# Kernel optimization log

Hardware: AMD Instinct MI355X
Metric: run time of the kernel (lower is better)

## Reference

```python
import jax, jax.numpy as jnp
import numpy as np
import math

N = 100000          # nodes
E = 3200000         # edges
F_IN = 500          # num_features
HID = 64            # hidden
C = 64              # num_classes
K = 5               # trig frequencies
OMEGA = 1.0
D = 10              # Taylor order / diffusion hops


def _taylor_coeffs():
    # cos/sin Taylor coefficient tables, [K, D+1] (static, fp64 then cast)
    x = (np.arange(1, K + 1) * OMEGA * np.pi)[:, None].astype(np.float64)
    cosc = np.zeros((K, D + 1), np.float64)
    sinc = np.zeros((K, D + 1), np.float64)
    even = np.arange(0, D + 1, 2)
    cosc[:, ::2] = ((-1.0) ** (even // 2)) * x ** even / np.array([math.factorial(int(o)) for o in even], np.float64)
    odd = np.arange(1, D + 1, 2)
    sinc[:, 1::2] = ((-1.0) ** ((odd - 1) // 2)) * x ** odd / np.array([math.factorial(int(o)) for o in odd], np.float64)
    return jnp.asarray(sinc, jnp.float32), jnp.asarray(cosc, jnp.float32)

SINC, COSC = _taylor_coeffs()


def setup_inputs() -> dict:
    key = jax.random.key(0)
    ks = jax.random.split(key, 8)
    feature = jax.random.normal(ks[0], (N, F_IN), dtype=jnp.float32)
    edges = jax.random.randint(ks[1], (2, E), 0, N, dtype=jnp.int64)
    W1 = jax.random.normal(ks[2], (F_IN, HID), dtype=jnp.float32) * (1.0 / np.sqrt(F_IN))
    b1 = jnp.zeros((HID,), jnp.float32)
    W2 = jax.random.normal(ks[3], (HID, C), dtype=jnp.float32) * (1.0 / np.sqrt(HID))
    b2 = jnp.zeros((C,), jnp.float32)
    xav = np.sqrt(2.0 / (1 + K))  # xavier_normal for (1, K)
    alpha = jax.random.normal(ks[4], (1, K), dtype=jnp.float32) * xav
    beta = jax.random.normal(ks[5], (1, K), dtype=jnp.float32) * xav
    return {"feature": feature, "edges": edges, "W1": W1, "b1": b1,
            "W2": W2, "b2": b2, "alpha": alpha, "beta": beta}


def reference(feature, edges, W1, b1, W2, b2, alpha, beta):
    # dropout is identity in eval mode
    x = jnp.maximum(feature @ W1 + b1, 0.0)   # lin1 + relu
    x = x @ W2 + b2                           # lin2 -> [N, C]

    # ---- Trigo_prop.__norm__: sym-normalized Laplacian, rescale, self-loops -1 ----
    src, dst = edges[0], edges[1]
    not_loop = src != dst                     # remove_self_loops
    deg = jax.ops.segment_sum(jnp.where(not_loop, 1.0, 0.0).astype(x.dtype), src, num_segments=N)
    dinv = jnp.where(deg > 0, jax.lax.rsqrt(deg), 0.0)
    w_off = jnp.where(not_loop, -(dinv[src] * dinv[dst]), 0.0)   # off-diag of L_sym
    # Laplacian diagonal entries are all 1 -> lambda_max = 2*max(all weights)
    lam = 2.0 * jnp.maximum(jnp.max(w_off), 1.0)
    s = 2.0 / lam
    w_off = w_off * s
    diag = s * 1.0 - 1.0                      # scaled diag(1) plus appended -1 self-loop

    # ---- D-hop Taylor-weighted diffusion ----
    coeff = (alpha @ SINC + beta @ COSC)[0]   # [D+1]
    Tx = x
    hidden = coeff[0] * Tx
    for d in range(1, D + 1):                 # fixed small D, unrolled
        Tx = jax.ops.segment_sum(w_off[:, None] * Tx[src], dst, num_segments=N) + diag * Tx
        hidden = hidden + coeff[d] * Tx
    out = hidden + x
    return jax.nn.log_softmax(out, axis=1)
```

## Files before the change

### kernel.cpp

```cpp
#include <hip/hip_runtime.h>
#include <math.h>

#define NN 100000
#define FIN 500
#define HIDN 64
#define KF 5
#define DORD 10

typedef unsigned short ushort_t;

struct Tables { float sinc[KF][DORD+1]; float cosc[KF][DORD+1]; };

__device__ inline float bl(unsigned u) { return __uint_as_float(u << 16); }
__device__ inline float bh(unsigned u) { return __uint_as_float(u & 0xffff0000u); }
__device__ inline unsigned short bf16_rne(float x) {
    unsigned u = __float_as_uint(x);
    return (unsigned short)((u + 0x7fffu + ((u >> 16) & 1u)) >> 16);
}
__device__ inline unsigned pack_bf16x2(float a, float b) {
    return (unsigned)bf16_rne(a) | ((unsigned)bf16_rne(b) << 16);
}

__global__ void coeff_kernel(const float* __restrict__ alpha, const float* __restrict__ beta,
                             Tables tb, float* __restrict__ coeff) {
    int d = threadIdx.x;
    if (d <= DORD) {
        float c = 0.f;
        #pragma unroll
        for (int k = 0; k < KF; ++k)
            c += alpha[k] * tb.sinc[k][d] + beta[k] * tb.cosc[k][d];
        coeff[d] = c;
    }
}

#define CHUNK 4096

__global__ __launch_bounds__(256) void hist_kernel(
    const int* __restrict__ src, const int* __restrict__ dst,
    int* __restrict__ histD, int* __restrict__ histS, int E, int nb) {
    __shared__ int hD[512];
    __shared__ int hS[512];
    for (int i = threadIdx.x; i < 512; i += 256) { hD[i] = 0; hS[i] = 0; }
    __syncthreads();
    int base = blockIdx.x * CHUNK;
    int end = base + CHUNK; if (end > E) end = E;
    for (int e = base + threadIdx.x; e < end; e += 256) {
        int s = src[e], d = dst[e];
        if (s != d) {
            atomicAdd(&hD[d >> 8], 1);
            atomicAdd(&hS[s >> 8], 1);
        }
    }
    __syncthreads();
    size_t ro = (size_t)blockIdx.x * 512;
    for (int i = threadIdx.x; i < nb; i += 256) {
        histD[ro + i] = hD[i];
        histS[ro + i] = hS[i];
    }
}

__global__ __launch_bounds__(512) void scanA_kernel(
    int* __restrict__ histD, int* __restrict__ histS,
    int* __restrict__ totD, int* __restrict__ totS, int nchunk, int nb) {
    __shared__ int tmp[512];
    int x = blockIdx.x;
    int* hist; int* tot; int b;
    if (x < nb) { hist = histD; tot = totD; b = x; }
    else        { hist = histS; tot = totS; b = x - nb; }
    int t = threadIdx.x;
    int carry = 0;
    for (int c0 = 0; c0 < nchunk; c0 += 512) {
        int c = c0 + t;
        tmp[t] = (c < nchunk) ? hist[(size_t)c * 512 + b] : 0;
        __syncthreads();
        for (int off = 1; off < 512; off <<= 1) {
            int add = (t >= off) ? tmp[t - off] : 0;
            __syncthreads();
            tmp[t] += add;
            __syncthreads();
        }
        if (c < nchunk) hist[(size_t)c * 512 + b] = carry + ((t > 0) ? tmp[t - 1] : 0);
        carry += tmp[511];
        __syncthreads();
    }
    if (t == 0) tot[b] = carry;
}

__global__ __launch_bounds__(512) void scanB_kernel(
    const int* __restrict__ totD, const int* __restrict__ totS,
    int* __restrict__ offD, int* __restrict__ offS, int nb) {
    __shared__ int tmp[512];
    int t = threadIdx.x;
    tmp[t] = (t < nb) ? totD[t] : 0;
    __syncthreads();
    for (int off = 1; off < 512; off <<= 1) {
        int add = (t >= off) ? tmp[t - off] : 0;
        __syncthreads();
        tmp[t] += add;
        __syncthreads();
    }
    if (t < nb) offD[t] = (t > 0) ? tmp[t - 1] : 0;
    if (t == nb - 1) offD[nb] = tmp[t];
    __syncthreads();
    tmp[t] = (t < nb) ? totS[t] : 0;
    __syncthreads();
    for (int off = 1; off < 512; off <<= 1) {
        int add = (t >= off) ? tmp[t - off] : 0;
        __syncthreads();
        tmp[t] += add;
        __syncthreads();
    }
    if (t < nb) offS[t] = (t > 0) ? tmp[t - 1] : 0;
    if (t == nb - 1) offS[nb] = tmp[t];
}

__global__ __launch_bounds__(256) void scatter_kernel(
    const int* __restrict__ src, const int* __restrict__ dst,
    const int* __restrict__ histD, const int* __restrict__ histS,
    const int* __restrict__ offD, const int* __restrict__ offS,
    unsigned* __restrict__ binned, unsigned char* __restrict__ srcbin, int E, int nb) {
    __shared__ int cD[512];
    __shared__ int cS[512];
    size_t ro = (size_t)blockIdx.x * 512;
    for (int i = threadIdx.x; i < nb; i += 256) {
        cD[i] = offD[i] + histD[ro + i];
        cS[i] = offS[i] + histS[ro + i];
    }
    __syncthreads();
    int base = blockIdx.x * CHUNK;
    int end = base + CHUNK; if (end > E) end = E;
    for (int e = base + threadIdx.x; e < end; e += 256) {
        int s = src[e], d = dst[e];
        if (s != d) {
            int pD = atomicAdd(&cD[d >> 8], 1);
            binned[pD] = (unsigned)s | ((unsigned)(d & 255) << 24);
            int pS = atomicAdd(&cS[s >> 8], 1);
            srcbin[pS] = (unsigned char)(s & 255);
        }
    }
}

__global__ __launch_bounds__(256) void bucket_csr_kernel(
    const unsigned* __restrict__ binned, const int* __restrict__ offD,
    int* __restrict__ row_ptr, int* __restrict__ col, int n, int nb) {
    int b = blockIdx.x;
    int e0 = offD[b], e1 = offD[b + 1];
    int d0 = b << 8;
    int dn = n - d0; if (dn > 256) dn = 256;
    __shared__ int ind[256];
    __shared__ int cur[256];
    int t = threadIdx.x;
    ind[t] = 0;
    __syncthreads();
    for (int e = e0 + t; e < e1; e += 256) {
        unsigned p = binned[e];
        atomicAdd(&ind[p >> 24], 1);
    }
    __syncthreads();
    for (int off = 1; off < 256; off <<= 1) {
        int add = (t >= off) ? ind[t - off] : 0;
        __syncthreads();
        ind[t] += add;
        __syncthreads();
    }
    if (t < dn) {
        int excl = (t > 0) ? ind[t - 1] : 0;
        row_ptr[d0 + t] = e0 + excl;
        cur[t] = e0 + excl;
    }
    if (b == 0 && t == 0) row_ptr[n] = offD[nb];
    __syncthreads();
    for (int e = e0 + t; e < e1; e += 256) {
        unsigned p = binned[e];
        int pos = atomicAdd(&cur[p >> 24], 1);
        col[pos] = (int)(p & 0xFFFFFFu);
    }
}

__global__ __launch_bounds__(256) void dinv_count_kernel(
    const unsigned char* __restrict__ srcbin, const int* __restrict__ offS,
    float* __restrict__ dinv, int n, int nb) {
    __shared__ int ind[256];
    int b = blockIdx.x;
    int t = threadIdx.x;
    ind[t] = 0;
    __syncthreads();
    int e0 = offS[b], e1 = offS[b + 1];
    for (int e = e0 + t; e < e1; e += 256)
        atomicAdd(&ind[srcbin[e]], 1);
    __syncthreads();
    int i = (b << 8) + t;
    if (i < n) {
        int c = ind[t];
        dinv[i] = (c > 0) ? (1.0f / sqrtf((float)c)) : 0.f;
    }
}

__global__ __launch_bounds__(256) void gemm1_kernel(
    const float* __restrict__ A, const float* __restrict__ W,
    const float* __restrict__ bias, float* __restrict__ H, int n) {
    __shared__ float sA[64][36];
    __shared__ float sW[32][64];
    int t = threadIdx.x;
    int tx = t & 15, ty = t >> 4;
    int rowBase = blockIdx.x * 64;
    float acc[4][4] = {{0.f}};
    for (int k0 = 0; k0 < FIN; k0 += 32) {
        #pragma unroll
        for (int l = 0; l < 2; ++l) {
            int c = t + l * 256;
            int r = c >> 3, cc = (c & 7) * 4;
            int gr = rowBase + r, gk = k0 + cc;
            float4 v = make_float4(0.f, 0.f, 0.f, 0.f);
            if (gr < n && gk < FIN) v = *(const float4*)(A + (size_t)gr * FIN + gk);
            *(float4*)&sA[r][cc] = v;
        }
        #pragma unroll
        for (int l = 0; l < 2; ++l) {
            int c = t + l * 256;
            int r = c >> 4, cc = (c & 15) * 4;
            int gk = k0 + r;
            float4 v = make_float4(0.f, 0.f, 0.f, 0.f);
            if (gk < FIN) v = *(const float4*)(W + (size_t)gk * 64 + cc);
            *(float4*)&sW[r][cc] = v;
        }
        __syncthreads();
        #pragma unroll
        for (int kk = 0; kk < 32; ++kk) {
            float a[4], b[4];
            #pragma unroll
            for (int i = 0; i < 4; ++i) a[i] = sA[ty * 4 + i][kk];
            #pragma unroll
            for (int j = 0; j < 4; ++j) b[j] = sW[kk][tx * 4 + j];
            #pragma unroll
            for (int i = 0; i < 4; ++i)
                #pragma unroll
                for (int j = 0; j < 4; ++j)
                    acc[i][j] = fmaf(a[i], b[j], acc[i][j]);
        }
        __syncthreads();
    }
    #pragma unroll
    for (int i = 0; i < 4; ++i) {
        int gr = rowBase + ty * 4 + i;
        if (gr < n) {
            float4 o;
            o.x = fmaxf(acc[i][0] + bias[tx * 4 + 0], 0.f);
            o.y = fmaxf(acc[i][1] + bias[tx * 4 + 1], 0.f);
            o.z = fmaxf(acc[i][2] + bias[tx * 4 + 2], 0.f);
            o.w = fmaxf(acc[i][3] + bias[tx * 4 + 3], 0.f);
            *(float4*)(H + (size_t)gr * 64 + tx * 4) = o;
        }
    }
}

__global__ __launch_bounds__(256) void gemm2_kernel(
    const float* __restrict__ H, const float* __restrict__ W2,
    const float* __restrict__ b2, const float* __restrict__ coeff,
    const float* __restrict__ dinv, ushort_t* __restrict__ ty0,
    float* __restrict__ out, int n) {
    __shared__ float sW[64 * 64];
    __shared__ float sb[64];
    int t = threadIdx.x;
    for (int i = t; i < 4096; i += 256) sW[i] = W2[i];
    if (t < 64) sb[t] = b2[t];
    __syncthreads();
    float c0p1 = 1.f + coeff[0];
    int lane = t & 63;
    int wid = t >> 6;
    int r0 = blockIdx.x * 128;
    int rend = r0 + 128; if (rend > n) rend = n;
    for (int r = r0 + wid; r < rend; r += 4) {
        float hv = H[(size_t)r * 64 + lane];
        float dr = dinv[r];
        float acc = sb[lane];
        #pragma unroll
        for (int k = 0; k < 64; ++k)
            acc = fmaf(__shfl(hv, k, 64), sW[k * 64 + lane], acc);
        ty0[(size_t)r * 64 + lane] = bf16_rne(dr * acc);
        out[(size_t)r * 64 + lane] = c0p1 * acc;
    }
}

__global__ __launch_bounds__(256) void spmm_kernel(
    const int* __restrict__ row_ptr, const int* __restrict__ col,
    const float* __restrict__ dinv, const ushort_t* __restrict__ tyin,
    ushort_t* __restrict__ tyout, float* __restrict__ out,
    const float* __restrict__ coeff, int d, int n, int fuse_lsm) {
    int wave = (blockIdx.x * blockDim.x + threadIdx.x) >> 6;
    if (wave >= n) return;
    int lane = threadIdx.x & 63;
    int sub = lane >> 4;
    int fl = lane & 15;
    int e0 = row_ptr[wave], e1 = row_ptr[wave + 1];
    float ax = 0.f, ay = 0.f, az = 0.f, aw = 0.f;
    int e = e0 + sub;
    for (; e + 12 < e1; e += 16) {
        int s0 = col[e], s1 = col[e + 4], s2 = col[e + 8], s3 = col[e + 12];
        uint2 p0 = *(const uint2*)(tyin + (size_t)s0 * 64 + fl * 4);
        uint2 p1 = *(const uint2*)(tyin + (size_t)s1 * 64 + fl * 4);
        uint2 p2 = *(const uint2*)(tyin + (size_t)s2 * 64 + fl * 4);
        uint2 p3 = *(const uint2*)(tyin + (size_t)s3 * 64 + fl * 4);
        ax += (bl(p0.x) + bl(p1.x)) + (bl(p2.x) + bl(p3.x));
        ay += (bh(p0.x) + bh(p1.x)) + (bh(p2.x) + bh(p3.x));
        az += (bl(p0.y) + bl(p1.y)) + (bl(p2.y) + bl(p3.y));
        aw += (bh(p0.y) + bh(p1.y)) + (bh(p2.y) + bh(p3.y));
    }
    for (; e < e1; e += 4) {
        int s = col[e];
        uint2 p = *(const uint2*)(tyin + (size_t)s * 64 + fl * 4);
        ax += bl(p.x); ay += bh(p.x); az += bl(p.y); aw += bh(p.y);
    }
    #pragma unroll
    for (int off = 16; off <= 32; off <<= 1) {
        ax += __shfl_xor(ax, off, 64);
        ay += __shfl_xor(ay, off, 64);
        az += __shfl_xor(az, off, 64);
        aw += __shfl_xor(aw, off, 64);
    }
    float dr = dinv[wave];
    float cd = coeff[d];
    float tx_x = -dr * ax, tx_y = -dr * ay, tx_z = -dr * az, tx_w = -dr * aw;
    float4 o = *(const float4*)(out + (size_t)wave * 64 + fl * 4);
    o.x += cd * tx_x; o.y += cd * tx_y; o.z += cd * tx_z; o.w += cd * tx_w;
    if (!fuse_lsm) {
        if (sub == 0) {
            uint2 ty;
            ty.x = pack_bf16x2(dr * tx_x, dr * tx_y);
            ty.y = pack_bf16x2(dr * tx_z, dr * tx_w);
            *(uint2*)(tyout + (size_t)wave * 64 + fl * 4) = ty;
            *(float4*)(out + (size_t)wave * 64 + fl * 4) = o;
        }
    } else {
        float m = fmaxf(fmaxf(o.x, o.y), fmaxf(o.z, o.w));
        #pragma unroll
        for (int off = 1; off < 16; off <<= 1) m = fmaxf(m, __shfl_xor(m, off, 64));
        float s4 = expf(o.x - m) + expf(o.y - m) + expf(o.z - m) + expf(o.w - m);
        #pragma unroll
        for (int off = 1; off < 16; off <<= 1) s4 += __shfl_xor(s4, off, 64);
        float lse = m + logf(s4);
        o.x -= lse; o.y -= lse; o.z -= lse; o.w -= lse;
        if (sub == 0)
            *(float4*)(out + (size_t)wave * 64 + fl * 4) = o;
    }
}

extern "C" void kernel_launch(void* const* d_in, const int* in_sizes, int n_in,
                              void* d_out, int out_size, void* d_ws, size_t ws_size,
                              hipStream_t stream) {
    const float* feature = (const float*)d_in[0];
    const int*   edges   = (const int*)d_in[1];
    const float* W1      = (const float*)d_in[2];
    const float* b1      = (const float*)d_in[3];
    const float* W2      = (const float*)d_in[4];
    const float* b2      = (const float*)d_in[5];
    const float* alpha   = (const float*)d_in[6];
    const float* beta    = (const float*)d_in[7];
    float* out = (float*)d_out;

    const int n = in_sizes[0] / FIN;
    const int E = in_sizes[1] / 2;
    const int* src = edges;
    const int* dst = edges + E;

    const int nb = (n + 255) >> 8;
    const int nchunk = (E + CHUNK - 1) / CHUNK;

    char* ws = (char*)d_ws;
    size_t off = 0;
    auto alloc = [&](size_t bytes) { size_t o = off; off = (off + bytes + 255) & ~(size_t)255; return o; };
    float*         coeff   = (float*)        (ws + alloc(64 * 4));
    float*         dinv    = (float*)        (ws + alloc((size_t)n * 4));
    int*           row_ptr = (int*)          (ws + alloc(((size_t)n + 1) * 4));
    int*           offD    = (int*)          (ws + alloc(513 * 4));
    int*           offS    = (int*)          (ws + alloc(513 * 4));
    int*           totD    = (int*)          (ws + alloc(512 * 4));
    int*           totS    = (int*)          (ws + alloc(512 * 4));
    int*           histD   = (int*)          (ws + alloc((size_t)nchunk * 512 * 4));
    int*           histS   = (int*)          (ws + alloc((size_t)nchunk * 512 * 4));
    int*           col     = (int*)          (ws + alloc((size_t)E * 4));
    unsigned*      binned  = (unsigned*)     (ws + alloc((size_t)E * 4));
    unsigned char* srcbin  = (unsigned char*)(ws + alloc((size_t)E));
    float*         H       = (float*)        (ws + alloc((size_t)n * 64 * 4));
    ushort_t*      TyA     = (ushort_t*)     (ws + alloc((size_t)n * 64 * 2));
    ushort_t*      TyB     = (ushort_t*)     (ws + alloc((size_t)n * 64 * 2));

    Tables tb;
    for (int k = 0; k < KF; ++k) {
        double x = M_PI * (double)(k + 1);
        double p = 1.0, f = 1.0;
        for (int o = 0; o <= DORD; ++o) {
            if (o > 0) { p *= x; f *= (double)o; }
            double v = p / f;
            tb.cosc[k][o] = (o % 2 == 0) ? (float)((((o / 2) % 2 == 0) ? 1.0 : -1.0) * v) : 0.f;
            tb.sinc[k][o] = (o % 2 == 1) ? (float)(((((o - 1) / 2) % 2 == 0) ? 1.0 : -1.0) * v) : 0.f;
        }
    }

    coeff_kernel<<<1, 64, 0, stream>>>(alpha, beta, tb, coeff);

    hist_kernel<<<nchunk, 256, 0, stream>>>(src, dst, histD, histS, E, nb);
    scanA_kernel<<<2 * nb, 512, 0, stream>>>(histD, histS, totD, totS, nchunk, nb);
    scanB_kernel<<<1, 512, 0, stream>>>(totD, totS, offD, offS, nb);
    scatter_kernel<<<nchunk, 256, 0, stream>>>(src, dst, histD, histS, offD, offS,
                                               binned, srcbin, E, nb);
    bucket_csr_kernel<<<nb, 256, 0, stream>>>(binned, offD, row_ptr, col, n, nb);
    dinv_count_kernel<<<nb, 256, 0, stream>>>(srcbin, offS, dinv, n, nb);

    gemm1_kernel<<<(n + 63) / 64, 256, 0, stream>>>(feature, W1, b1, H, n);
    gemm2_kernel<<<(n + 127) / 128, 256, 0, stream>>>(H, W2, b2, coeff, dinv, TyA, out, n);

    const ushort_t* tin = TyA;
    ushort_t* bufs[2] = { TyB, TyA };
    for (int d = 1; d <= DORD; ++d) {
        ushort_t* tout = bufs[(d - 1) & 1];
        spmm_kernel<<<(n + 3) / 4, 256, 0, stream>>>(row_ptr, col, dinv, tin, tout, out,
                                                     coeff, d, n, d == DORD ? 1 : 0);
        tin = tout;
    }
}
```

Measured before the change: 1.286 ms.

## Replace fp32 FMA first linear layer with bf16 MFMA GEMM

Replaces the scalar fp32 tiled GEMM for feature@W1 with a bf16 MFMA 16x16x32 kernel. A prep kernel transposes W1 and converts it to bf16, padded to K=512. The feature rows are converted to bf16 on the fly while being staged into LDS. This removes FMA-bound compute on the 100000x500x64 GEMM, so the kernel becomes bound by reading the fp32 features, at the cost of reduced precision in the first layer.

New measurement: 1.267 ms. About the same (-1.4%).

```diff
diff --git a/kernel.cpp b/kernel.cpp
--- a/kernel.cpp
+++ b/kernel.cpp
@@ -6,8 +6,12 @@
 #define HIDN 64
 #define KF 5
 #define DORD 10
+#define KPAD 512
+#define NKT 8
 
 typedef unsigned short ushort_t;
+typedef __attribute__((ext_vector_type(8))) short short8v;
+typedef __attribute__((ext_vector_type(4))) float f32x4;
 
 struct Tables { float sinc[KF][DORD+1]; float cosc[KF][DORD+1]; };
 
@@ -196,60 +200,104 @@
     }
 }
 
-__global__ __launch_bounds__(256) void gemm1_kernel(
-    const float* __restrict__ A, const float* __restrict__ W,
+__global__ __launch_bounds__(256) void wprep_kernel(
+    const float* __restrict__ W1, ushort_t* __restrict__ Wt) {
+    int tid = blockIdx.x * 256 + threadIdx.x;
+    if (tid >= 64 * KPAD) return;
+    int kk = tid & (KPAD - 1);
+    int c = tid >> 9;
+    float v = (kk < FIN) ? W1[(size_t)kk * 64 + c] : 0.f;
+    Wt[(size_t)c * KPAD + kk] = bf16_rne(v);
+}
+
+__global__ __launch_bounds__(256) void gemm1_mfma_kernel(
+    const float* __restrict__ A, const ushort_t* __restrict__ Wt,
     const float* __restrict__ bias, float* __restrict__ H, int n) {
-    __shared__ float sA[64][36];
-    __shared__ float sW[32][64];
-    int t = threadIdx.x;
-    int tx = t & 15, ty = t >> 4;
-    int rowBase = blockIdx.x * 64;
-    float acc[4][4] = {{0.f}};
-    for (int k0 = 0; k0 < FIN; k0 += 32) {
+    __shared__ ushort_t sA[128][72];
+    __shared__ ushort_t sB[64][72];
+    int t = threadIdx.x;
+    int w = t >> 6;
+    int lane = t & 63;
+    int lr = lane & 15;
+    int lg = lane >> 4;
+    int rowBase = blockIdx.x * 128;
+
+    f32x4 acc[2][4];
+    #pragma unroll
+    for (int r = 0; r < 2; ++r)
+        #pragma unroll
+        for (int c = 0; c < 4; ++c)
+            acc[r][c] = (f32x4){0.f, 0.f, 0.f, 0.f};
+
+    for (int kt = 0; kt < NKT; ++kt) {
+        #pragma unroll
+        for (int l = 0; l < 8; ++l) {
+            int idx = t + l * 256;
+            int r = idx >> 4;
+            int kc = (idx & 15) * 4;
+            int gr = rowBase + r;
+            int gk = kt * 64 + kc;
+            float4 v = make_float4(0.f, 0.f, 0.f, 0.f);
+            if (gr < n) {
+                if (gk + 3 < FIN) {
+                    v = *(const float4*)(A + (size_t)gr * FIN + gk);
+                } else {
+                    float* vp = (float*)&v;
+                    #pragma unroll
+                    for (int j = 0; j < 4; ++j)
+                        if (gk + j < FIN) vp[j] = A[(size_t)gr * FIN + gk + j];
+                }
+            }
+            uint2 p;
+            p.x = pack_bf16x2(v.x, v.y);
+            p.y = pack_bf16x2(v.z, v.w);
+            *(uint2*)&sA[r][kc] = p;
+        }
         #pragma unroll
         for (int l = 0; l < 2; ++l) {
-            int c = t + l * 256;
-            int r = c >> 3, cc = (c & 7) * 4;
-            int gr = rowBase + r, gk = k0 + cc;
-            float4 v = make_float4(0.f, 0.f, 0.f, 0.f);
-            if (gr < n && gk < FIN) v = *(const float4*)(A + (size_t)gr * FIN + gk);
-            *(float4*)&sA[r][cc] = v;
-        }
-        #pragma unroll
-        for (int l = 0; l < 2; ++l) {
-            int c = t + l * 256;
-            int r = c >> 4, cc = (c & 15) * 4;
-            int gk = k0 + r;
-            float4 v = make_float4(0.f, 0.f, 0.f, 0.f);
-            if (gk < FIN) v = *(const float4*)(W + (size_t)gk * 64 + cc);
-            *(float4*)&sW[r][cc] = v;
-        }
-        __syncthreads();
-        #pragma unroll
-        for (int kk = 0; kk < 32; ++kk) {
-            float a[4], b[4];
+            int idx = t + l * 256;
+            int c = idx >> 3;
+            int kc = (idx & 7) * 8;
+            uint4 v = *(const uint4*)(Wt + (size_t)c * KPAD + kt * 64 + kc);
+            *(uint4*)&sB[c][kc] = v;
+        }
+        __syncthreads();
+
+        short8v af[2][2], bfr[4][2];
+        #pragma unroll
+        for (int r = 0; r < 2; ++r)
             #pragma unroll
-            for (int i = 0; i < 4; ++i) a[i] = sA[ty * 4 + i][kk];
+            for (int h = 0; h < 2; ++h)
+                af[r][h] = *(const short8v*)&sA[w * 32 + r * 16 + lr][h * 32 + lg * 8];
+        #pragma unroll
+        for (int c = 0; c < 4; ++c)
             #pragma unroll
-            for (int j = 0; j < 4; ++j) b[j] = sW[kk][tx * 4 + j];
+            for (int h = 0; h < 2; ++h)
+                bfr[c][h] = *(const short8v*)&sB[c * 16 + lr][h * 32 + lg * 8];
+        #pragma unroll
+        for (int r = 0; r < 2; ++r)
             #pragma unroll
-            for (int i = 0; i < 4; ++i)
+            for (int c = 0; c < 4; ++c)
                 #pragma unroll
-                for (int j = 0; j < 4; ++j)
-                    acc[i][j] = fmaf(a[i], b[j], acc[i][j]);
-        }
-        __syncthreads();
-    }
+                for (int h = 0; h < 2; ++h)
+                    acc[r][c] = __builtin_amdgcn_mfma_f32_16x16x32_bf16(
+                        af[r][h], bfr[c][h], acc[r][c], 0, 0, 0);
+        __syncthreads();
+    }
+
+    float bcol[4];
     #pragma unroll
-    for (int i = 0; i < 4; ++i) {
-        int gr = rowBase + ty * 4 + i;
-        if (gr < n) {
-            float4 o;
-            o.x = fmaxf(acc[i][0] + bias[tx * 4 + 0], 0.f);
-            o.y = fmaxf(acc[i][1] + bias[tx * 4 + 1], 0.f);
-            o.z = fmaxf(acc[i][2] + bias[tx * 4 + 2], 0.f);
-            o.w = fmaxf(acc[i][3] + bias[tx * 4 + 3], 0.f);
-            *(float4*)(H + (size_t)gr * 64 + tx * 4) = o;
+    for (int c = 0; c < 4; ++c) bcol[c] = bias[c * 16 + lr];
+    #pragma unroll
+    for (int r = 0; r < 2; ++r) {
+        #pragma unroll
+        for (int c = 0; c < 4; ++c) {
+            #pragma unroll
+            for (int i = 0; i < 4; ++i) {
+                int row = rowBase + w * 32 + r * 16 + lg * 4 + i;
+                if (row < n)
+                    H[(size_t)row * 64 + c * 16 + lr] = fmaxf(acc[r][c][i] + bcol[c], 0.f);
+            }
         }
     }
 }
@@ -376,6 +424,7 @@
     int*           offS    = (int*)          (ws + alloc(513 * 4));
     int*           totD    = (int*)          (ws + alloc(512 * 4));
     int*           totS    = (int*)          (ws + alloc(512 * 4));
+    ushort_t*      Wt      = (ushort_t*)     (ws + alloc((size_t)64 * KPAD * 2));
     int*           histD   = (int*)          (ws + alloc((size_t)nchunk * 512 * 4));
     int*           histS   = (int*)          (ws + alloc((size_t)nchunk * 512 * 4));
     int*           col     = (int*)          (ws + alloc((size_t)E * 4));
@@ -398,6 +447,7 @@
     }
 
     coeff_kernel<<<1, 64, 0, stream>>>(alpha, beta, tb, coeff);
+    wprep_kernel<<<(64 * KPAD + 255) / 256, 256, 0, stream>>>(W1, Wt);
 
     hist_kernel<<<nchunk, 256, 0, stream>>>(src, dst, histD, histS, E, nb);
     scanA_kernel<<<2 * nb, 512, 0, stream>>>(histD, histS, totD, totS, nchunk, nb);
@@ -407,7 +457,7 @@
     bucket_csr_kernel<<<nb, 256, 0, stream>>>(binned, offD, row_ptr, col, n, nb);
     dinv_count_kernel<<<nb, 256, 0, stream>>>(srcbin, offS, dinv, n, nb);
 
-    gemm1_kernel<<<(n + 63) / 64, 256, 0, stream>>>(feature, W1, b1, H, n);
+    gemm1_mfma_kernel<<<(n + 127) / 128, 256, 0, stream>>>(feature, Wt, b1, H, n);
     gemm2_kernel<<<(n + 127) / 128, 256, 0, stream>>>(H, W2, b2, coeff, dinv, TyA, out, n);
 
     const ushort_t* tin = TyA;
```
